# Kernel optimization log

Hardware: AMD Instinct MI355X
Metric: run time of the kernel (lower is better)

The kernel has to match this reference:

```python
import jax, jax.numpy as jnp
import numpy as np

B, L, XS, YS, A, C, NL = 32, 4096, 256, 256, 4, 64, 5  # batch, seq, x_size, y_size, n_actions, hid_cnn, cnn_layers


def _conv2d(x, w):
    # x: [N,Cin,H,W], w: [Cout,Cin,3,3], stride 1, pad 1 ('SAME')
    return jax.lax.conv_general_dilated(x, w, (1, 1), 'SAME',
                                        dimension_numbers=('NCHW', 'OIHW', 'NCHW'))


def setup_inputs() -> dict:
    key = jax.random.key(0)
    ks = jax.random.split(key, 16)
    stdv = 1.0 / np.sqrt(XS)
    inp = {
        'x': jax.random.normal(ks[0], (B, L, XS), jnp.float32),
        'y': jax.random.normal(ks[1], (B, YS), jnp.float32),
        'x_mask': jax.random.randint(ks[2], (B, L), 0, 2) == 1,
        'actions': jax.random.randint(ks[3], (B,), 0, A),
        'weight': jax.random.uniform(ks[4], (YS, XS), jnp.float32, -stdv, stdv),
    }
    chans = [(1, C)] + [(C, C)] * (NL - 2) + [(C, 1)]
    for i, (ci, co) in enumerate(chans):
        bound = 1.0 / np.sqrt(ci * 9)
        inp[f'cw{i}'] = jax.random.uniform(ks[5 + 2 * i], (A, co, ci, 3, 3), jnp.float32, -bound, bound)
        inp[f'cb{i}'] = jax.random.uniform(ks[6 + 2 * i], (A, co), jnp.float32, -bound, bound)
    return inp


def reference(x, y, x_mask, actions, weight,
              cw0, cb0, cw1, cb1, cw2, cb2, cw3, cb3, cw4, cb4):
    img = weight[None, None]  # [1,1,YS,XS] -- weight matrix as a 1-channel image

    def per_action(w0, b0, w1, b1, w2, b2, w3, b3, w4, b4):
        out = img
        layers = ((w0, b0), (w1, b1), (w2, b2), (w3, b3), (w4, b4))
        for i, (w, b) in enumerate(layers):
            out = _conv2d(out, w) + b[None, :, None, None]
            if i < NL - 1:
                out = jax.nn.relu(out)
        return out[0, 0]  # [YS,XS]

    # all per-action conv stacks batched via vmap -> [A,YS,XS]
    W_a = jax.vmap(per_action)(cw0, cb0, cw1, cb1, cw2, cb2, cw3, cb3, cw4, cb4)
    # one-hot multiply + sum over actions == select the per-sample action matrix
    Wy = jnp.einsum('bh,bhx->bx', y, W_a[actions])          # [B,XS]
    xWy = jnp.einsum('blx,bx->bl', x, Wy)                   # [B,L]
    xWy = jnp.where(x_mask, -jnp.inf, xWy)
    return jax.nn.softmax(xWy, axis=-1)  # eval-mode output (training uses log_softmax)
```

## Files before the change

### kernel.cpp

```cpp
#include <hip/hip_runtime.h>
#include <cstdint>
#include <cstddef>

typedef __attribute__((ext_vector_type(8))) short bf16x8;
typedef __attribute__((ext_vector_type(4))) float f32x4;
typedef __attribute__((ext_vector_type(4))) int i32x4;

__device__ inline unsigned short cvt_bf16_rne(float f) {
    unsigned u = __builtin_bit_cast(unsigned, f);
    u = (u + 0x7FFFu + ((u >> 16) & 1u)) >> 16;
    return (unsigned short)u;
}
__device__ inline float bf16_to_f32(unsigned short s) {
    return __builtin_bit_cast(float, (unsigned)s << 16);
}

__global__ void clear_flag_kernel(int* flag) {
    if (threadIdx.x == 0) *flag = 0;
}

__global__ void detect_mask_kernel(const unsigned int* m, int* flag) {
    int i = blockIdx.x * blockDim.x + threadIdx.x;
    int f = 0;
    #pragma unroll
    for (int k = 0; k < 4; ++k) {
        unsigned int v = m[i * 4 + k];
        if (v == 0x3F800000u) f |= 2;
        else if (v > 1u) f |= 1;
    }
    if (f) atomicOr(flag, f);
}

__global__ void apack_kernel(const float* __restrict__ cw, char* __restrict__ apack) {
    int t = threadIdx.x;
    int tap = blockIdx.x, a = blockIdx.y;
    int ks = t >> 8, mf = (t >> 6) & 3, lane = t & 63;
    int n = lane & 15, q = lane >> 4;
    int co = mf * 16 + n;
    int ci0 = ks * 32 + q * 8;
    unsigned d[4];
    #pragma unroll
    for (int jj = 0; jj < 4; ++jj) {
        unsigned short h0 = cvt_bf16_rne(cw[((size_t)(a * 64 + co) * 64 + ci0 + 2 * jj + 0) * 9 + tap]);
        unsigned short h1 = cvt_bf16_rne(cw[((size_t)(a * 64 + co) * 64 + ci0 + 2 * jj + 1) * 9 + tap]);
        d[jj] = (unsigned)h0 | ((unsigned)h1 << 16);
    }
    *(i32x4*)(apack + ((((size_t)(a * 9 + tap) * 2 + ks) * 4 + mf) * 1024 + lane * 16)) =
        *(i32x4*)d;
}

__global__ void conv_first_kernel(const float* __restrict__ img,
                                  const float* __restrict__ cw0,
                                  const float* __restrict__ cb0,
                                  unsigned short* __restrict__ act) {
    int y = blockIdx.x, a = blockIdx.y, x = threadIdx.x;
    float p[3][3];
    #pragma unroll
    for (int ty = 0; ty < 3; ++ty)
        #pragma unroll
        for (int tx = 0; tx < 3; ++tx) {
            int py = y + ty - 1, px = x + tx - 1;
            p[ty][tx] = ((unsigned)py < 256u && (unsigned)px < 256u)
                        ? img[py * 256 + px] : 0.0f;
        }
    const float* w = cw0 + (size_t)a * 64 * 9;
    const float* b = cb0 + a * 64;
    unsigned pk[32];
    #pragma unroll
    for (int co = 0; co < 64; ++co) {
        const float* wc = w + co * 9;
        float acc = b[co];
        #pragma unroll
        for (int ty = 0; ty < 3; ++ty)
            #pragma unroll
            for (int tx = 0; tx < 3; ++tx)
                acc = fmaf(wc[ty * 3 + tx], p[ty][tx], acc);
        acc = fmaxf(acc, 0.0f);
        unsigned short hv = cvt_bf16_rne(acc);
        if (co & 1) pk[co >> 1] |= ((unsigned)hv << 16);
        else        pk[co >> 1] = (unsigned)hv;
    }
    char* ob = (char*)act + (((size_t)(a << 16) + (y << 8) + x) << 7);
    #pragma unroll
    for (int k = 0; k < 8; ++k)
        *(i32x4*)(ob + k * 16) = *(i32x4*)&pk[k * 4];
}

__global__ __launch_bounds__(256, 3)
void conv_mid_mfma(const unsigned short* __restrict__ act_in,
                   const char* __restrict__ apack_l,
                   const float* __restrict__ cb,
                   unsigned short* __restrict__ act_out) {
    __shared__ i32x4 lds4[340 * 9];
    int tid = threadIdx.x;
    int a = blockIdx.z;
    int r0 = blockIdx.y * 8, c0 = blockIdx.x * 32;
    const char* actb = (const char*)act_in;

    for (int s = tid; s < 2720; s += 256) {
        int px = s >> 3, o = s & 7;
        int prow = px / 34, pcol = px - prow * 34;
        int grow = r0 - 1 + prow, gcol = c0 - 1 + pcol;
        i32x4 v = {0, 0, 0, 0};
        if ((unsigned)grow < 256u && (unsigned)gcol < 256u)
            v = *(const i32x4*)(actb + (((size_t)(a << 16) + (grow << 8) + gcol) << 7) + (o << 4));
        lds4[px * 9 + o] = v;
    }
    __syncthreads();

    int lane = tid & 63, wv = tid >> 6;
    int n = lane & 15, q = lane >> 4;

    f32x4 acc[4][4];
    #pragma unroll
    for (int mf = 0; mf < 4; ++mf) {
        f32x4 bb = *(const f32x4*)(cb + a * 64 + mf * 16 + q * 4);
        #pragma unroll
        for (int nf = 0; nf < 4; ++nf) acc[mf][nf] = bb;
    }

    int base_nf[4];
    #pragma unroll
    for (int nf = 0; nf < 4; ++nf) {
        int orl = wv * 2 + (nf >> 1);
        int ocl = ((nf & 1) << 4) + n;
        base_nf[nf] = (orl * 34 + ocl) * 9 + q;
    }
    const char* ap = apack_l + (size_t)a * 9 * 8192 + lane * 16;

    #pragma unroll
    for (int tap = 0; tap < 9; ++tap) {
        const int ty = tap / 3, tx = tap - ty * 3;
        const int toff = (ty * 34 + tx) * 9;
        #pragma unroll
        for (int ks = 0; ks < 2; ++ks) {
            bf16x8 Af[4], Bf[4];
            #pragma unroll
            for (int mf = 0; mf < 4; ++mf)
                Af[mf] = __builtin_bit_cast(bf16x8,
                    *(const i32x4*)(ap + (((tap * 2 + ks) * 4 + mf) << 10)));
            #pragma unroll
            for (int nf = 0; nf < 4; ++nf)
                Bf[nf] = __builtin_bit_cast(bf16x8, lds4[base_nf[nf] + toff + ks * 4]);
            #pragma unroll
            for (int mf = 0; mf < 4; ++mf)
                #pragma unroll
                for (int nf = 0; nf < 4; ++nf)
                    acc[mf][nf] = __builtin_amdgcn_mfma_f32_16x16x32_bf16(
                        Af[mf], Bf[nf], acc[mf][nf], 0, 0, 0);
        }
    }

    #pragma unroll
    for (int nf = 0; nf < 4; ++nf) {
        int grow = r0 + wv * 2 + (nf >> 1);
        int gcol = c0 + ((nf & 1) << 4) + n;
        char* ob = (char*)act_out + (((size_t)(a << 16) + (grow << 8) + gcol) << 7) + q * 8;
        #pragma unroll
        for (int mf = 0; mf < 4; ++mf) {
            f32x4 v = acc[mf][nf];
            unsigned d0 = (unsigned)cvt_bf16_rne(fmaxf(v.x, 0.0f))
                        | ((unsigned)cvt_bf16_rne(fmaxf(v.y, 0.0f)) << 16);
            unsigned d1 = (unsigned)cvt_bf16_rne(fmaxf(v.z, 0.0f))
                        | ((unsigned)cvt_bf16_rne(fmaxf(v.w, 0.0f)) << 16);
            uint2 st; st.x = d0; st.y = d1;
            *(uint2*)(ob + mf * 32) = st;
        }
    }
}

__global__ void conv_last_kernel(const unsigned short* __restrict__ act,
                                 const float* __restrict__ cw4,
                                 const float* __restrict__ cb4,
                                 float* __restrict__ W_a) {
    int y = blockIdx.x, a = blockIdx.y;
    int tid = threadIdx.x;
    int lane = tid & 63, wv = tid >> 6;
    int o = lane & 7, pl = lane >> 3;
    float wr[8][9];
    #pragma unroll
    for (int j = 0; j < 8; ++j) {
        const float* wp = cw4 + ((size_t)a * 64 + o * 8 + j) * 9;
        #pragma unroll
        for (int t = 0; t < 9; ++t) wr[j][t] = wp[t];
    }
    const char* actb = (const char*)act;
    float bias = cb4[a];
    for (int i = 0; i < 8; ++i) {
        int x = i * 32 + wv * 8 + pl;
        float p = 0.0f;
        #pragma unroll
        for (int ty = 0; ty < 3; ++ty) {
            int py = y + ty - 1;
            #pragma unroll
            for (int tx = 0; tx < 3; ++tx) {
                int px = x + tx - 1;
                if ((unsigned)py < 256u && (unsigned)px < 256u) {
                    i32x4 v = *(const i32x4*)(actb +
                        (((size_t)(a << 16) + (py << 8) + px) << 7) + (o << 4));
                    const unsigned* dv = (const unsigned*)&v;
                    #pragma unroll
                    for (int j = 0; j < 8; ++j) {
                        unsigned d = dv[j >> 1];
                        unsigned short us = (j & 1) ? (unsigned short)(d >> 16)
                                                    : (unsigned short)(d & 0xffffu);
                        p = fmaf(bf16_to_f32(us), wr[j][ty * 3 + tx], p);
                    }
                }
            }
        }
        p += __shfl_xor(p, 1, 64);
        p += __shfl_xor(p, 2, 64);
        p += __shfl_xor(p, 4, 64);
        if (o == 0) W_a[(size_t)(a << 16) + (y << 8) + x] = p + bias;
    }
}

__global__ void wy_kernel(const float* __restrict__ yv,
                          const int* __restrict__ actions,
                          const float* __restrict__ W_a,
                          float* __restrict__ Wy) {
    int b = blockIdx.x, x = threadIdx.x;
    int a = actions[b];
    const float* Wp = W_a + (size_t)a * 65536;
    const float* yb = yv + b * 256;
    float acc = 0.0f;
    #pragma unroll 8
    for (int h = 0; h < 256; ++h)
        acc = fmaf(yb[h], Wp[(size_t)h * 256 + x], acc);
    Wy[b * 256 + x] = acc;
}

__global__ void logits_kernel(const float* __restrict__ xv,
                              const void* __restrict__ mask,
                              const int* __restrict__ flag,
                              const float* __restrict__ Wy,
                              float* __restrict__ out) {
    int tid = threadIdx.x, lane = tid & 63, wave = tid >> 6;
    int b = blockIdx.y;
    int fl = *flag;
    float4 wy4 = *(const float4*)(Wy + b * 256 + lane * 4);
    const float* xb = xv + (size_t)b * 4096 * 256;
    int l0 = blockIdx.x * 128 + wave * 32;
    for (int li = 0; li < 32; ++li) {
        int l = l0 + li;
        const float4 x4 = *(const float4*)(xb + (size_t)l * 256 + lane * 4);
        float p = x4.x * wy4.x + x4.y * wy4.y + x4.z * wy4.z + x4.w * wy4.w;
        #pragma unroll
        for (int off = 32; off > 0; off >>= 1)
            p += __shfl_xor(p, off, 64);
        if (lane == 0) {
            size_t mi = (size_t)b * 4096 + l;
            bool msk;
            if (fl & 2)      msk = ((const float*)mask)[mi] != 0.0f;
            else if (fl & 1) msk = ((const unsigned char*)mask)[mi] != 0;
            else             msk = ((const int*)mask)[mi] != 0;
            out[mi] = msk ? -__builtin_inff() : p;
        }
    }
}

__global__ void softmax_kernel(float* __restrict__ out) {
    int b = blockIdx.x, tid = threadIdx.x;
    int lane = tid & 63, wid = tid >> 6;
    float* row = out + (size_t)b * 4096;
    float v[4];
    float m = -__builtin_inff();
    #pragma unroll
    for (int i = 0; i < 4; ++i) { v[i] = row[tid + i * 1024]; m = fmaxf(m, v[i]); }
    #pragma unroll
    for (int off = 32; off > 0; off >>= 1) m = fmaxf(m, __shfl_xor(m, off, 64));
    __shared__ float redm[16];
    __shared__ float reds[16];
    if (lane == 0) redm[wid] = m;
    __syncthreads();
    float M = redm[0];
    #pragma unroll
    for (int j = 1; j < 16; ++j) M = fmaxf(M, redm[j]);
    float s = 0.0f;
    #pragma unroll
    for (int i = 0; i < 4; ++i) { v[i] = expf(v[i] - M); s += v[i]; }
    #pragma unroll
    for (int off = 32; off > 0; off >>= 1) s += __shfl_xor(s, off, 64);
    if (lane == 0) reds[wid] = s;
    __syncthreads();
    float S = 0.0f;
    #pragma unroll
    for (int j = 0; j < 16; ++j) S += reds[j];
    float inv = 1.0f / S;
    #pragma unroll
    for (int i = 0; i < 4; ++i) row[tid + i * 1024] = v[i] * inv;
}

extern "C" void kernel_launch(void* const* d_in, const int* in_sizes, int n_in,
                              void* d_out, int out_size, void* d_ws, size_t ws_size,
                              hipStream_t stream) {
    const float* xv      = (const float*)d_in[0];
    const float* yv      = (const float*)d_in[1];
    const void*  xmask   = d_in[2];
    const int*   actions = (const int*)d_in[3];
    const float* weight  = (const float*)d_in[4];
    const float* cw0 = (const float*)d_in[5];
    const float* cb0 = (const float*)d_in[6];
    const float* cw1 = (const float*)d_in[7];
    const float* cb1 = (const float*)d_in[8];
    const float* cw2 = (const float*)d_in[9];
    const float* cb2 = (const float*)d_in[10];
    const float* cw3 = (const float*)d_in[11];
    const float* cb3 = (const float*)d_in[12];
    const float* cw4 = (const float*)d_in[13];
    const float* cb4 = (const float*)d_in[14];
    float* out = (float*)d_out;

    char* ws = (char*)d_ws;
    unsigned short* bufA = (unsigned short*)ws;
    unsigned short* bufB = (unsigned short*)(ws + 33554432);
    char*  apack = ws + 67108864;
    float* W_a   = (float*)(ws + 67993600);
    float* Wy    = (float*)(ws + 69042176);
    int*   flag  = (int*)(ws + 69074944);

    clear_flag_kernel<<<1, 64, 0, stream>>>(flag);
    detect_mask_kernel<<<32, 256, 0, stream>>>((const unsigned int*)xmask, flag);

    apack_kernel<<<dim3(9, 4), 512, 0, stream>>>(cw1, apack);
    apack_kernel<<<dim3(9, 4), 512, 0, stream>>>(cw2, apack + 294912);
    apack_kernel<<<dim3(9, 4), 512, 0, stream>>>(cw3, apack + 589824);

    conv_first_kernel<<<dim3(256, 4), 256, 0, stream>>>(weight, cw0, cb0, bufA);
    conv_mid_mfma<<<dim3(8, 32, 4), 256, 0, stream>>>(bufA, apack,          cb1, bufB);
    conv_mid_mfma<<<dim3(8, 32, 4), 256, 0, stream>>>(bufB, apack + 294912, cb2, bufA);
    conv_mid_mfma<<<dim3(8, 32, 4), 256, 0, stream>>>(bufA, apack + 589824, cb3, bufB);
    conv_last_kernel<<<dim3(256, 4), 256, 0, stream>>>(bufB, cw4, cb4, W_a);

    wy_kernel<<<32, 256, 0, stream>>>(yv, actions, W_a, Wy);
    logits_kernel<<<dim3(32, 32), 256, 0, stream>>>(xv, xmask, flag, Wy, out);
    softmax_kernel<<<32, 1024, 0, stream>>>(out);
}
```

Before: 404.0 us.

## Fuse first conv into first MFMA conv, merge weight packing, batch logit rows

The 1→64 channel first convolution is now computed per tile directly into shared memory inside the first MFMA conv kernel, recomputing the halo. This removes the separate kernel and the full bf16 activation write and read round-trip through global memory. The three weight-packing launches and the flag-clear launch are merged into one kernel. The logits kernel handles four rows per iteration, interleaving their shuffle reductions and writing float4 outputs. The cost is redundant first-layer work on halo pixels and more register pressure in the fused kernel.

Measured after the change: 362.9 us. 10.2% less time.

```diff
diff --git a/kernel.cpp b/kernel.cpp
--- a/kernel.cpp
+++ b/kernel.cpp
@@ -15,10 +15,6 @@
     return __builtin_bit_cast(float, (unsigned)s << 16);
 }
 
-__global__ void clear_flag_kernel(int* flag) {
-    if (threadIdx.x == 0) *flag = 0;
-}
-
 __global__ void detect_mask_kernel(const unsigned int* m, int* flag) {
     int i = blockIdx.x * blockDim.x + threadIdx.x;
     int f = 0;
@@ -31,9 +27,16 @@
     if (f) atomicOr(flag, f);
 }
 
-__global__ void apack_kernel(const float* __restrict__ cw, char* __restrict__ apack) {
+__global__ void apack_all_kernel(const float* __restrict__ cw1,
+                                 const float* __restrict__ cw2,
+                                 const float* __restrict__ cw3,
+                                 char* __restrict__ apack,
+                                 int* __restrict__ flag) {
     int t = threadIdx.x;
-    int tap = blockIdx.x, a = blockIdx.y;
+    int tap = blockIdx.x, a = blockIdx.y, lz = blockIdx.z;
+    if (tap == 0 && a == 0 && lz == 0 && t == 0) *flag = 0;
+    const float* cw = (lz == 0) ? cw1 : (lz == 1 ? cw2 : cw3);
+    char* outp = apack + (size_t)lz * 294912;
     int ks = t >> 8, mf = (t >> 6) & 3, lane = t & 63;
     int n = lane & 15, q = lane >> 4;
     int co = mf * 16 + n;
@@ -45,45 +48,74 @@
         unsigned short h1 = cvt_bf16_rne(cw[((size_t)(a * 64 + co) * 64 + ci0 + 2 * jj + 1) * 9 + tap]);
         d[jj] = (unsigned)h0 | ((unsigned)h1 << 16);
     }
-    *(i32x4*)(apack + ((((size_t)(a * 9 + tap) * 2 + ks) * 4 + mf) * 1024 + lane * 16)) =
+    *(i32x4*)(outp + ((((size_t)(a * 9 + tap) * 2 + ks) * 4 + mf) * 1024 + lane * 16)) =
         *(i32x4*)d;
 }
 
-__global__ void conv_first_kernel(const float* __restrict__ img,
-                                  const float* __restrict__ cw0,
-                                  const float* __restrict__ cb0,
-                                  unsigned short* __restrict__ act) {
-    int y = blockIdx.x, a = blockIdx.y, x = threadIdx.x;
-    float p[3][3];
-    #pragma unroll
-    for (int ty = 0; ty < 3; ++ty)
-        #pragma unroll
-        for (int tx = 0; tx < 3; ++tx) {
-            int py = y + ty - 1, px = x + tx - 1;
-            p[ty][tx] = ((unsigned)py < 256u && (unsigned)px < 256u)
-                        ? img[py * 256 + px] : 0.0f;
-        }
-    const float* w = cw0 + (size_t)a * 64 * 9;
-    const float* b = cb0 + a * 64;
-    unsigned pk[32];
-    #pragma unroll
-    for (int co = 0; co < 64; ++co) {
-        const float* wc = w + co * 9;
-        float acc = b[co];
-        #pragma unroll
-        for (int ty = 0; ty < 3; ++ty)
-            #pragma unroll
-            for (int tx = 0; tx < 3; ++tx)
-                acc = fmaf(wc[ty * 3 + tx], p[ty][tx], acc);
-        acc = fmaxf(acc, 0.0f);
-        unsigned short hv = cvt_bf16_rne(acc);
-        if (co & 1) pk[co >> 1] |= ((unsigned)hv << 16);
-        else        pk[co >> 1] = (unsigned)hv;
-    }
-    char* ob = (char*)act + (((size_t)(a << 16) + (y << 8) + x) << 7);
-    #pragma unroll
-    for (int k = 0; k < 8; ++k)
-        *(i32x4*)(ob + k * 16) = *(i32x4*)&pk[k * 4];
+__device__ __forceinline__ void conv_mid_body(const i32x4* lds4,
+                                              const char* __restrict__ apack_l,
+                                              const float* __restrict__ cb,
+                                              unsigned short* __restrict__ act_out,
+                                              int a, int r0, int c0, int tid) {
+    int lane = tid & 63, wv = tid >> 6;
+    int n = lane & 15, q = lane >> 4;
+
+    f32x4 acc[4][4];
+    #pragma unroll
+    for (int mf = 0; mf < 4; ++mf) {
+        f32x4 bb = *(const f32x4*)(cb + a * 64 + mf * 16 + q * 4);
+        #pragma unroll
+        for (int nf = 0; nf < 4; ++nf) acc[mf][nf] = bb;
+    }
+
+    int base_nf[4];
+    #pragma unroll
+    for (int nf = 0; nf < 4; ++nf) {
+        int orl = wv * 2 + (nf >> 1);
+        int ocl = ((nf & 1) << 4) + n;
+        base_nf[nf] = (orl * 34 + ocl) * 9 + q;
+    }
+    const char* ap = apack_l + (size_t)a * 9 * 8192 + lane * 16;
+
+    #pragma unroll
+    for (int tap = 0; tap < 9; ++tap) {
+        const int ty = tap / 3, tx = tap - ty * 3;
+        const int toff = (ty * 34 + tx) * 9;
+        #pragma unroll
+        for (int ks = 0; ks < 2; ++ks) {
+            bf16x8 Af[4], Bf[4];
+            #pragma unroll
+            for (int mf = 0; mf < 4; ++mf)
+                Af[mf] = __builtin_bit_cast(bf16x8,
+                    *(const i32x4*)(ap + (((tap * 2 + ks) * 4 + mf) << 10)));
+            #pragma unroll
+            for (int nf = 0; nf < 4; ++nf)
+                Bf[nf] = __builtin_bit_cast(bf16x8, lds4[base_nf[nf] + toff + ks * 4]);
+            #pragma unroll
+            for (int mf = 0; mf < 4; ++mf)
+                #pragma unroll
+                for (int nf = 0; nf < 4; ++nf)
+                    acc[mf][nf] = __builtin_amdgcn_mfma_f32_16x16x32_bf16(
+                        Af[mf], Bf[nf], acc[mf][nf], 0, 0, 0);
+        }
+    }
+
+    #pragma unroll
+    for (int nf = 0; nf < 4; ++nf) {
+        int grow = r0 + wv * 2 + (nf >> 1);
+        int gcol = c0 + ((nf & 1) << 4) + n;
+        char* ob = (char*)act_out + (((size_t)(a << 16) + (grow << 8) + gcol) << 7) + q * 8;
+        #pragma unroll
+        for (int mf = 0; mf < 4; ++mf) {
+            f32x4 v = acc[mf][nf];
+            unsigned d0 = (unsigned)cvt_bf16_rne(fmaxf(v.x, 0.0f))
+                        | ((unsigned)cvt_bf16_rne(fmaxf(v.y, 0.0f)) << 16);
+            unsigned d1 = (unsigned)cvt_bf16_rne(fmaxf(v.z, 0.0f))
+                        | ((unsigned)cvt_bf16_rne(fmaxf(v.w, 0.0f)) << 16);
+            uint2 st; st.x = d0; st.y = d1;
+            *(uint2*)(ob + mf * 32) = st;
+        }
+    }
 }
 
 __global__ __launch_bounds__(256, 3)
@@ -107,66 +139,70 @@
         lds4[px * 9 + o] = v;
     }
     __syncthreads();
-
-    int lane = tid & 63, wv = tid >> 6;
-    int n = lane & 15, q = lane >> 4;
-
-    f32x4 acc[4][4];
-    #pragma unroll
-    for (int mf = 0; mf < 4; ++mf) {
-        f32x4 bb = *(const f32x4*)(cb + a * 64 + mf * 16 + q * 4);
-        #pragma unroll
-        for (int nf = 0; nf < 4; ++nf) acc[mf][nf] = bb;
-    }
-
-    int base_nf[4];
-    #pragma unroll
-    for (int nf = 0; nf < 4; ++nf) {
-        int orl = wv * 2 + (nf >> 1);
-        int ocl = ((nf & 1) << 4) + n;
-        base_nf[nf] = (orl * 34 + ocl) * 9 + q;
-    }
-    const char* ap = apack_l + (size_t)a * 9 * 8192 + lane * 16;
-
-    #pragma unroll
-    for (int tap = 0; tap < 9; ++tap) {
-        const int ty = tap / 3, tx = tap - ty * 3;
-        const int toff = (ty * 34 + tx) * 9;
-        #pragma unroll
-        for (int ks = 0; ks < 2; ++ks) {
-            bf16x8 Af[4], Bf[4];
-            #pragma unroll
-            for (int mf = 0; mf < 4; ++mf)
-                Af[mf] = __builtin_bit_cast(bf16x8,
-                    *(const i32x4*)(ap + (((tap * 2 + ks) * 4 + mf) << 10)));
-            #pragma unroll
-            for (int nf = 0; nf < 4; ++nf)
-                Bf[nf] = __builtin_bit_cast(bf16x8, lds4[base_nf[nf] + toff + ks * 4]);
-            #pragma unroll
-            for (int mf = 0; mf < 4; ++mf)
+    conv_mid_body(lds4, apack_l, cb, act_out, a, r0, c0, tid);
+}
+
+__global__ __launch_bounds__(256, 3)
+void conv_mid_fused0(const float* __restrict__ img,
+                     const float* __restrict__ cw0,
+                     const float* __restrict__ cb0,
+                     const char* __restrict__ apack_l,
+                     const float* __restrict__ cb,
+                     unsigned short* __restrict__ act_out) {
+    __shared__ i32x4 lds4[340 * 9];
+    __shared__ float img_s[12 * 36];
+    int tid = threadIdx.x;
+    int a = blockIdx.z;
+    int r0 = blockIdx.y * 8, c0 = blockIdx.x * 32;
+
+    for (int s = tid; s < 432; s += 256) {
+        int ir = s / 36, ic = s - ir * 36;
+        int gr = r0 - 2 + ir, gc = c0 - 2 + ic;
+        img_s[s] = ((unsigned)gr < 256u && (unsigned)gc < 256u) ? img[gr * 256 + gc] : 0.0f;
+    }
+    __syncthreads();
+
+    int o = tid & 7;
+    float wr[8][9], br[8];
+    #pragma unroll
+    for (int j = 0; j < 8; ++j) {
+        const float* wp = cw0 + ((size_t)a * 64 + o * 8 + j) * 9;
+        #pragma unroll
+        for (int t = 0; t < 9; ++t) wr[j][t] = wp[t];
+        br[j] = cb0[a * 64 + o * 8 + j];
+    }
+
+    for (int s = tid; s < 2720; s += 256) {
+        int px = s >> 3;
+        int prow = px / 34, pcol = px - prow * 34;
+        int grow = r0 - 1 + prow, gcol = c0 - 1 + pcol;
+        i32x4 v = {0, 0, 0, 0};
+        if ((unsigned)grow < 256u && (unsigned)gcol < 256u) {
+            float accv[8];
+            #pragma unroll
+            for (int j = 0; j < 8; ++j) accv[j] = br[j];
+            #pragma unroll
+            for (int dy = 0; dy < 3; ++dy)
                 #pragma unroll
-                for (int nf = 0; nf < 4; ++nf)
-                    acc[mf][nf] = __builtin_amdgcn_mfma_f32_16x16x32_bf16(
-                        Af[mf], Bf[nf], acc[mf][nf], 0, 0, 0);
-        }
-    }
-
-    #pragma unroll
-    for (int nf = 0; nf < 4; ++nf) {
-        int grow = r0 + wv * 2 + (nf >> 1);
-        int gcol = c0 + ((nf & 1) << 4) + n;
-        char* ob = (char*)act_out + (((size_t)(a << 16) + (grow << 8) + gcol) << 7) + q * 8;
-        #pragma unroll
-        for (int mf = 0; mf < 4; ++mf) {
-            f32x4 v = acc[mf][nf];
-            unsigned d0 = (unsigned)cvt_bf16_rne(fmaxf(v.x, 0.0f))
-                        | ((unsigned)cvt_bf16_rne(fmaxf(v.y, 0.0f)) << 16);
-            unsigned d1 = (unsigned)cvt_bf16_rne(fmaxf(v.z, 0.0f))
-                        | ((unsigned)cvt_bf16_rne(fmaxf(v.w, 0.0f)) << 16);
-            uint2 st; st.x = d0; st.y = d1;
-            *(uint2*)(ob + mf * 32) = st;
-        }
-    }
+                for (int dx = 0; dx < 3; ++dx) {
+                    float iv = img_s[(prow + dy) * 36 + (pcol + dx)];
+                    #pragma unroll
+                    for (int j = 0; j < 8; ++j)
+                        accv[j] = fmaf(wr[j][dy * 3 + dx], iv, accv[j]);
+                }
+            unsigned d[4];
+            #pragma unroll
+            for (int jj = 0; jj < 4; ++jj) {
+                unsigned short h0 = cvt_bf16_rne(fmaxf(accv[2 * jj + 0], 0.0f));
+                unsigned short h1 = cvt_bf16_rne(fmaxf(accv[2 * jj + 1], 0.0f));
+                d[jj] = (unsigned)h0 | ((unsigned)h1 << 16);
+            }
+            v = *(i32x4*)d;
+        }
+        lds4[px * 9 + o] = v;
+    }
+    __syncthreads();
+    conv_mid_body(lds4, apack_l, cb, act_out, a, r0, c0, tid);
 }
 
 __global__ void conv_last_kernel(const unsigned short* __restrict__ act,
@@ -242,20 +278,49 @@
     float4 wy4 = *(const float4*)(Wy + b * 256 + lane * 4);
     const float* xb = xv + (size_t)b * 4096 * 256;
     int l0 = blockIdx.x * 128 + wave * 32;
-    for (int li = 0; li < 32; ++li) {
+    float ninf = -__builtin_inff();
+    for (int li = 0; li < 32; li += 4) {
         int l = l0 + li;
-        const float4 x4 = *(const float4*)(xb + (size_t)l * 256 + lane * 4);
-        float p = x4.x * wy4.x + x4.y * wy4.y + x4.z * wy4.z + x4.w * wy4.w;
-        #pragma unroll
-        for (int off = 32; off > 0; off >>= 1)
-            p += __shfl_xor(p, off, 64);
+        const float* rp = xb + (size_t)l * 256 + lane * 4;
+        float4 x0 = *(const float4*)(rp);
+        float4 x1 = *(const float4*)(rp + 256);
+        float4 x2 = *(const float4*)(rp + 512);
+        float4 x3 = *(const float4*)(rp + 768);
+        float p0 = x0.x * wy4.x + x0.y * wy4.y + x0.z * wy4.z + x0.w * wy4.w;
+        float p1 = x1.x * wy4.x + x1.y * wy4.y + x1.z * wy4.z + x1.w * wy4.w;
+        float p2 = x2.x * wy4.x + x2.y * wy4.y + x2.z * wy4.z + x2.w * wy4.w;
+        float p3 = x3.x * wy4.x + x3.y * wy4.y + x3.z * wy4.z + x3.w * wy4.w;
+        #pragma unroll
+        for (int off = 32; off > 0; off >>= 1) {
+            p0 += __shfl_xor(p0, off, 64);
+            p1 += __shfl_xor(p1, off, 64);
+            p2 += __shfl_xor(p2, off, 64);
+            p3 += __shfl_xor(p3, off, 64);
+        }
         if (lane == 0) {
             size_t mi = (size_t)b * 4096 + l;
-            bool msk;
-            if (fl & 2)      msk = ((const float*)mask)[mi] != 0.0f;
-            else if (fl & 1) msk = ((const unsigned char*)mask)[mi] != 0;
-            else             msk = ((const int*)mask)[mi] != 0;
-            out[mi] = msk ? -__builtin_inff() : p;
+            float4 r;
+            r.x = p0; r.y = p1; r.z = p2; r.w = p3;
+            if (fl & 2) {
+                const float* mp = (const float*)mask + mi;
+                if (mp[0] != 0.0f) r.x = ninf;
+                if (mp[1] != 0.0f) r.y = ninf;
+                if (mp[2] != 0.0f) r.z = ninf;
+                if (mp[3] != 0.0f) r.w = ninf;
+            } else if (fl & 1) {
+                const unsigned char* mp = (const unsigned char*)mask + mi;
+                if (mp[0]) r.x = ninf;
+                if (mp[1]) r.y = ninf;
+                if (mp[2]) r.z = ninf;
+                if (mp[3]) r.w = ninf;
+            } else {
+                const int* mp = (const int*)mask + mi;
+                if (mp[0]) r.x = ninf;
+                if (mp[1]) r.y = ninf;
+                if (mp[2]) r.z = ninf;
+                if (mp[3]) r.w = ninf;
+            }
+            *(float4*)(out + mi) = r;
         }
     }
 }
@@ -320,18 +385,13 @@
     float* Wy    = (float*)(ws + 69042176);
     int*   flag  = (int*)(ws + 69074944);
 
-    clear_flag_kernel<<<1, 64, 0, stream>>>(flag);
+    apack_all_kernel<<<dim3(9, 4, 3), 512, 0, stream>>>(cw1, cw2, cw3, apack, flag);
     detect_mask_kernel<<<32, 256, 0, stream>>>((const unsigned int*)xmask, flag);
 
-    apack_kernel<<<dim3(9, 4), 512, 0, stream>>>(cw1, apack);
-    apack_kernel<<<dim3(9, 4), 512, 0, stream>>>(cw2, apack + 294912);
-    apack_kernel<<<dim3(9, 4), 512, 0, stream>>>(cw3, apack + 589824);
-
-    conv_first_kernel<<<dim3(256, 4), 256, 0, stream>>>(weight, cw0, cb0, bufA);
-    conv_mid_mfma<<<dim3(8, 32, 4), 256, 0, stream>>>(bufA, apack,          cb1, bufB);
-    conv_mid_mfma<<<dim3(8, 32, 4), 256, 0, stream>>>(bufB, apack + 294912, cb2, bufA);
-    conv_mid_mfma<<<dim3(8, 32, 4), 256, 0, stream>>>(bufA, apack + 589824, cb3, bufB);
-    conv_last_kernel<<<dim3(256, 4), 256, 0, stream>>>(bufB, cw4, cb4, W_a);
+    conv_mid_fused0<<<dim3(8, 32, 4), 256, 0, stream>>>(weight, cw0, cb0, apack, cb1, bufA);
+    conv_mid_mfma<<<dim3(8, 32, 4), 256, 0, stream>>>(bufA, apack + 294912, cb2, bufB);
+    conv_mid_mfma<<<dim3(8, 32, 4), 256, 0, stream>>>(bufB, apack + 589824, cb3, bufA);
+    conv_last_kernel<<<dim3(256, 4), 256, 0, stream>>>(bufA, cw4, cb4, W_a);
 
     wy_kernel<<<32, 256, 0, stream>>>(yv, actions, W_a, Wy);
     logits_kernel<<<dim3(32, 32), 256, 0, stream>>>(xv, xmask, flag, Wy, out);
```
